# Kernel tuning notes

Hardware: AMD Instinct MI355X
Metric: run time of the kernel (lower is better)

The kernel has to match this reference:

```python
import jax, jax.numpy as jnp
import numpy as np

N = 4
SEGMENTS = 16
IN_F = 256
OUT_F = 256
BATCH = 512


def chebyshev_lobatto(n):
    # Chebyshev-Lobatto interpolation nodes on [-1, 1]
    k = jnp.arange(n, dtype=jnp.float32)
    return -jnp.cos(jnp.pi * k / (n - 1))


def lagrange_basis(x, nodes):
    # x: [B, In]; returns basis values [B, In, n]
    n = nodes.shape[0]
    cols = []
    for j in range(n):  # n is a small static constant (4)
        terms = [(x - nodes[m]) / (nodes[j] - nodes[m]) for m in range(n) if m != j]
        cols.append(jnp.prod(jnp.stack(terms, axis=0), axis=0))
    return jnp.stack(cols, axis=-1)


def setup_inputs() -> dict:
    key = jax.random.key(0)
    k1, k2 = jax.random.split(key)
    x = jax.random.uniform(k1, (BATCH, IN_F), dtype=jnp.float32, minval=-1.0, maxval=1.0)
    w = jax.random.uniform(
        k2, (OUT_F, IN_F, (N - 1) * SEGMENTS + 1), dtype=jnp.float32, minval=-1.0, maxval=1.0
    )
    return {"x": x, "w": w, "n": N, "segments": SEGMENTS}


def reference(x, w, n, segments):
    nodes = chebyshev_lobatto(n)
    # segment id per element, clamped to [0, segments-1]
    id_min = jnp.clip(((x + 1.0) / 2.0 * segments).astype(jnp.int32), 0, segments - 1)
    id_max = id_min + 1
    wid_min = id_min * (n - 1)  # start of weight slice; slice length == n
    # segment boundaries in x-space: eta(i) = i/segments * 2 - 1
    x_min = id_min.astype(x.dtype) / segments * 2.0 - 1.0
    x_max = id_max.astype(x.dtype) / segments * 2.0 - 1.0
    # rescale x into [-1, 1] within its segment
    x_in = 2.0 * (x - x_min) / (x_max - x_min) - 1.0
    basis = lagrange_basis(x_in, nodes)  # [B, In, n]
    # gather per-element weight slice: w_g[b,i,j,o] = w[o, i, wid_min[b,i]+j]
    idx = wid_min[..., None] + jnp.arange(n)  # [B, In, n]
    w_t = jnp.transpose(w, (1, 2, 0))  # [In, K, Out]
    in_f = w.shape[1]
    w_g = w_t[jnp.arange(in_f)[None, :, None], idx]  # [B, In, n, Out]
    # interpolate and sum over in_features (matches einsum 'ijk,jkli->jl')
    return jnp.einsum("bin,bino->bo", basis, w_g)
```

## Files before the change

kernel.cpp:

```cpp
#include <hip/hip_runtime.h>


typedef _Float16 h2 __attribute__((ext_vector_type(2)));

#define INF     256
#define OUTF    256
#define WSTRIDE 49
#define OSTRIDE (INF * WSTRIDE)
#define NSPLIT  32
#define IPB     8
#define WE_UINTS (256 * 256 * 32)

#define GLOAD16(gptr, lptr)                                                         \
  __builtin_amdgcn_global_load_lds(                                                 \
      (const __attribute__((address_space(1))) unsigned int*)(gptr),                \
      (__attribute__((address_space(3))) unsigned int*)(lptr), 16, 0, 0)

__global__ __launch_bounds__(256)
void pp_expand(const float* __restrict__ w, unsigned int* __restrict__ we) {
    const int i = blockIdx.x;
    const int o = threadIdx.x;
    const float* src = w + (size_t)o * OSTRIDE + i * WSTRIDE;
    float t[49];
    #pragma unroll
    for (int k = 0; k < 49; ++k) t[k] = src[k];
    unsigned int pk[32];
    #pragma unroll
    for (int s = 0; s < 16; ++s) {
        auto p0 = __builtin_amdgcn_cvt_pkrtz(t[3*s],   t[3*s+1]);
        auto p1 = __builtin_amdgcn_cvt_pkrtz(t[3*s+2], t[3*s+3]);
        pk[2*s]   = __builtin_bit_cast(unsigned int, p0);
        pk[2*s+1] = __builtin_bit_cast(unsigned int, p1);
    }
    uint4* dst = (uint4*)(we + ((size_t)i * 256 + o) * 32);
    #pragma unroll
    for (int k = 0; k < 8; ++k)
        dst[k] = make_uint4(pk[4*k], pk[4*k+1], pk[4*k+2], pk[4*k+3]);
}

#define STAGE(ci)                                                                   \
do {                                                                                \
    unsigned int* lds_ = &smem[((ci) & 1) * 4096];                                  \
    _Pragma("unroll")                                                               \
    for (int it = 0; it < 4; ++it) {                                                \
        int f_ = it * 256 + tid;                            \
        int iloc_ = f_ >> 9;                                                        \
        int rem_  = f_ & 511;                                                       \
        const unsigned int* gp_ = we + ((size_t)(i_base + (ci)*2 + iloc_) * 256     \
                                        + o_base) * 32 + rem_ * 4;                  \
        GLOAD16(gp_, lds_ + f_ * 4);                                                \
    }                                                                               \
} while (0)

#define COMPUTE(ci)                                                                 \
do {                                                                                \
    _Pragma("unroll")                                                               \
    for (int il = 0; il < 2; ++il) {                                                \
        const int ig_ = (ci) * 2 + il;                                              \
        const unsigned int* p_ = &smem[((ci) & 1) * 4096                            \
                                       + (il * 64 + o_off) * 32 + sseg[ig_] * 2];   \
        const h2 cA_ = ch01[ig_], cB_ = ch23[ig_];                                  \
        _Pragma("unroll")                                                           \
        for (int oo = 0; oo < 16; ++oo) {                                           \
            uint2 v_ = *(const uint2*)(p_ + oo * 32);                               \
            acc[oo] = __builtin_amdgcn_fdot2(__builtin_bit_cast(h2, v_.x), cA_,     \
                                             acc[oo], false);                       \
            acc[oo] = __builtin_amdgcn_fdot2(__builtin_bit_cast(h2, v_.y), cB_,     \
                                             acc[oo], false);                       \
        }                                                                           \
    }                                                                               \
} while (0)

__global__ __launch_bounds__(256, 4)
void pp_partial(const float* __restrict__ x, const unsigned int* __restrict__ we,
                float* __restrict__ part) {
    __shared__ unsigned int smem[8192];

    const int tid  = threadIdx.x;
    const int wave = tid >> 6, lane = tid & 63;
    const int isplit = blockIdx.x;
    const int i_base = isplit * IPB;
    const int o_base = blockIdx.y * 64;
    const int b_base = blockIdx.z * 64;
    const int b = b_base + lane;
    const int o_off = wave * 16;

    int sseg[IPB];
    h2  ch01[IPB], ch23[IPB];
    {
        const float4* xp = (const float4*)(x + (size_t)b * INF + i_base);
        float4 x0 = xp[0], x1 = xp[1];
        float xs[8] = {x0.x, x0.y, x0.z, x0.w, x1.x, x1.y, x1.z, x1.w};
        #pragma unroll
        for (int i = 0; i < IPB; ++i) {
            float xx = xs[i];
            int id = (int)((xx + 1.0f) * 8.0f);
            id = id < 0 ? 0 : (id > 15 ? 15 : id);
            float u = (xx - ((float)id * 0.125f - 1.0f)) * 16.0f - 1.0f;
            float a = u + 1.0f, b2 = u + 0.5f, cc = u - 0.5f, d = u - 1.0f;
            float c0 = b2 * cc * d  * (-2.0f / 3.0f);
            float c1 = a  * cc * d  * ( 4.0f / 3.0f);
            float c2 = a  * b2 * d  * (-4.0f / 3.0f);
            float c3 = a  * b2 * cc * ( 2.0f / 3.0f);
            h2 pA; pA[0] = (_Float16)c0; pA[1] = (_Float16)c1;
            h2 pB; pB[0] = (_Float16)c2; pB[1] = (_Float16)c3;
            ch01[i] = pA; ch23[i] = pB;
            sseg[i] = id;
        }
    }

    float acc[16];
    #pragma unroll
    for (int q = 0; q < 16; ++q) acc[q] = 0.0f;

    STAGE(0);
    __syncthreads();
    STAGE(1); COMPUTE(0); __syncthreads();
    STAGE(2); COMPUTE(1); __syncthreads();
    STAGE(3); COMPUTE(2); __syncthreads();
    COMPUTE(3);

    float4* wp = (float4*)(part + (size_t)isplit * (512 * 256)
                                + (size_t)b * 256 + o_base + o_off);
    #pragma unroll
    for (int q = 0; q < 4; ++q)
        wp[q] = make_float4(acc[4*q], acc[4*q+1], acc[4*q+2], acc[4*q+3]);
}

__global__ __launch_bounds__(256)
void pp_reduce(const float* __restrict__ part, float* __restrict__ out) {
    const size_t off = (size_t)blockIdx.x * 256 + threadIdx.x;
    float s = 0.0f;
    #pragma unroll
    for (int k = 0; k < NSPLIT; ++k)
        s += part[(size_t)k * (512 * 256) + off];
    out[off] = s;
}

extern "C" void kernel_launch(void* const* d_in, const int* in_sizes, int n_in,
                              void* d_out, int out_size, void* d_ws, size_t ws_size,
                              hipStream_t stream) {
    const float* x = (const float*)d_in[0];
    const float* w = (const float*)d_in[1];
    float* out = (float*)d_out;
    unsigned int* we = (unsigned int*)d_ws;
    float* part = (float*)((char*)d_ws + (size_t)WE_UINTS * 4);
    (void)ws_size; (void)n_in; (void)in_sizes; (void)out_size;

    pp_expand<<<dim3(256), 256, 0, stream>>>(w, we);
    pp_partial<<<dim3(NSPLIT, 4, 8), 256, 0, stream>>>(x, we, part);
    pp_reduce<<<dim3(512), 256, 0, stream>>>(part, out);
}
```

Before: 91.75 us.

## Interleave output pairs in fp16 weight layout and load whole tile once

The expand kernel now stores weights with two adjacent outputs interleaved per segment, so each compute lane reads one 16-byte LDS vector that serves two outputs. The partial kernel drops the double-buffered staging pipeline and loads all 8 inputs' weights for 32 outputs at once. It then transposes the accumulators through LDS so the partial-sum stores are coalesced. The grid doubles in the output dimension, and the reduce kernel is vectorised to float4. The change trades the load/compute overlap for fewer LDS instructions and better store coalescing.

```diff
diff --git a/kernel.cpp b/kernel.cpp
--- a/kernel.cpp
+++ b/kernel.cpp
@@ -9,7 +9,7 @@
 #define OSTRIDE (INF * WSTRIDE)
 #define NSPLIT  32
 #define IPB     8
-#define WE_UINTS (256 * 256 * 32)
+#define WE_UINTS (256 * 128 * 64)
 
 #define GLOAD16(gptr, lptr)                                                         \
   __builtin_amdgcn_global_load_lds(                                                 \
@@ -24,52 +24,18 @@
     float t[49];
     #pragma unroll
     for (int k = 0; k < 49; ++k) t[k] = src[k];
-    unsigned int pk[32];
+    const int op = o >> 1, e = o & 1;
+    unsigned int* dst = we + ((size_t)i * 128 + op) * 64 + e * 2;
     #pragma unroll
     for (int s = 0; s < 16; ++s) {
         auto p0 = __builtin_amdgcn_cvt_pkrtz(t[3*s],   t[3*s+1]);
         auto p1 = __builtin_amdgcn_cvt_pkrtz(t[3*s+2], t[3*s+3]);
-        pk[2*s]   = __builtin_bit_cast(unsigned int, p0);
-        pk[2*s+1] = __builtin_bit_cast(unsigned int, p1);
+        uint2 v;
+        v.x = __builtin_bit_cast(unsigned int, p0);
+        v.y = __builtin_bit_cast(unsigned int, p1);
+        *(uint2*)(dst + s * 4) = v;
     }
-    uint4* dst = (uint4*)(we + ((size_t)i * 256 + o) * 32);
-    #pragma unroll
-    for (int k = 0; k < 8; ++k)
-        dst[k] = make_uint4(pk[4*k], pk[4*k+1], pk[4*k+2], pk[4*k+3]);
 }
-
-#define STAGE(ci)                                                                   \
-do {                                                                                \
-    unsigned int* lds_ = &smem[((ci) & 1) * 4096];                                  \
-    _Pragma("unroll")                                                               \
-    for (int it = 0; it < 4; ++it) {                                                \
-        int f_ = it * 256 + tid;                            \
-        int iloc_ = f_ >> 9;                                                        \
-        int rem_  = f_ & 511;                                                       \
-        const unsigned int* gp_ = we + ((size_t)(i_base + (ci)*2 + iloc_) * 256     \
-                                        + o_base) * 32 + rem_ * 4;                  \
-        GLOAD16(gp_, lds_ + f_ * 4);                                                \
-    }                                                                               \
-} while (0)
-
-#define COMPUTE(ci)                                                                 \
-do {                                                                                \
-    _Pragma("unroll")                                                               \
-    for (int il = 0; il < 2; ++il) {                                                \
-        const int ig_ = (ci) * 2 + il;                                              \
-        const unsigned int* p_ = &smem[((ci) & 1) * 4096                            \
-                                       + (il * 64 + o_off) * 32 + sseg[ig_] * 2];   \
-        const h2 cA_ = ch01[ig_], cB_ = ch23[ig_];                                  \
-        _Pragma("unroll")                                                           \
-        for (int oo = 0; oo < 16; ++oo) {                                           \
-            uint2 v_ = *(const uint2*)(p_ + oo * 32);                               \
-            acc[oo] = __builtin_amdgcn_fdot2(__builtin_bit_cast(h2, v_.x), cA_,     \
-                                             acc[oo], false);                       \
-            acc[oo] = __builtin_amdgcn_fdot2(__builtin_bit_cast(h2, v_.y), cB_,     \
-                                             acc[oo], false);                       \
-        }                                                                           \
-    }                                                                               \
-} while (0)
 
 __global__ __launch_bounds__(256, 4)
 void pp_partial(const float* __restrict__ x, const unsigned int* __restrict__ we,
@@ -78,15 +44,23 @@
 
     const int tid  = threadIdx.x;
     const int wave = tid >> 6, lane = tid & 63;
-    const int isplit = blockIdx.x;
-    const int i_base = isplit * IPB;
-    const int o_base = blockIdx.y * 64;
-    const int b_base = blockIdx.z * 64;
+    const int isplit  = blockIdx.x;
+    const int i_base  = isplit * IPB;
+    const int op_base = blockIdx.y * 16;
+    const int o_base  = blockIdx.y * 32;
+    const int b_base  = blockIdx.z * 64;
     const int b = b_base + lane;
-    const int o_off = wave * 16;
 
-    int sseg[IPB];
-    h2  ch01[IPB], ch23[IPB];
+    #pragma unroll
+    for (int it = 0; it < 8; ++it) {
+        int u = it * 256 + tid;
+        int iloc = u >> 8, opl = (u >> 4) & 15, s = u & 15;
+        const unsigned int* gp =
+            we + (((size_t)(i_base + iloc) * 128 + op_base + opl) * 16 + s) * 4;
+        GLOAD16(gp, &smem[u * 4]);
+    }
+
+    int sseg[IPB]; h2 cA[IPB], cB[IPB];
     {
         const float4* xp = (const float4*)(x + (size_t)b * INF + i_base);
         float4 x0 = xp[0], x1 = xp[1];
@@ -104,37 +78,66 @@
             float c3 = a  * b2 * cc * ( 2.0f / 3.0f);
             h2 pA; pA[0] = (_Float16)c0; pA[1] = (_Float16)c1;
             h2 pB; pB[0] = (_Float16)c2; pB[1] = (_Float16)c3;
-            ch01[i] = pA; ch23[i] = pB;
-            sseg[i] = id;
+            cA[i] = pA; cB[i] = pB; sseg[i] = id;
         }
     }
 
-    float acc[16];
+    __syncthreads();
+
+    float acc[8];
     #pragma unroll
-    for (int q = 0; q < 16; ++q) acc[q] = 0.0f;
+    for (int q = 0; q < 8; ++q) acc[q] = 0.0f;
 
-    STAGE(0);
+    #pragma unroll
+    for (int i = 0; i < IPB; ++i) {
+        const unsigned int* p = &smem[(i * 16 + wave * 4) * 64 + sseg[i] * 4];
+        #pragma unroll
+        for (int pq = 0; pq < 4; ++pq) {
+            uint4 v = *(const uint4*)(p + pq * 64);
+            acc[2*pq]   = __builtin_amdgcn_fdot2(__builtin_bit_cast(h2, v.x), cA[i],
+                                                 acc[2*pq],   false);
+            acc[2*pq]   = __builtin_amdgcn_fdot2(__builtin_bit_cast(h2, v.y), cB[i],
+                                                 acc[2*pq],   false);
+            acc[2*pq+1] = __builtin_amdgcn_fdot2(__builtin_bit_cast(h2, v.z), cA[i],
+                                                 acc[2*pq+1], false);
+            acc[2*pq+1] = __builtin_amdgcn_fdot2(__builtin_bit_cast(h2, v.w), cB[i],
+                                                 acc[2*pq+1], false);
+        }
+    }
+
     __syncthreads();
-    STAGE(1); COMPUTE(0); __syncthreads();
-    STAGE(2); COMPUTE(1); __syncthreads();
-    STAGE(3); COMPUTE(2); __syncthreads();
-    COMPUTE(3);
+    float* smf = (float*)smem;
+    #pragma unroll
+    for (int q = 0; q < 8; ++q)
+        smf[lane * 33 + wave * 8 + q] = acc[q];
+    __syncthreads();
 
-    float4* wp = (float4*)(part + (size_t)isplit * (512 * 256)
-                                + (size_t)b * 256 + o_base + o_off);
+    const int qo = tid & 7;
+    const int g  = tid >> 3;
     #pragma unroll
-    for (int q = 0; q < 4; ++q)
-        wp[q] = make_float4(acc[4*q], acc[4*q+1], acc[4*q+2], acc[4*q+3]);
+    for (int r = 0; r < 2; ++r) {
+        int b_l = g + 32 * r;
+        float4 v;
+        v.x = smf[b_l * 33 + qo * 4 + 0];
+        v.y = smf[b_l * 33 + qo * 4 + 1];
+        v.z = smf[b_l * 33 + qo * 4 + 2];
+        v.w = smf[b_l * 33 + qo * 4 + 3];
+        *(float4*)(part + (size_t)isplit * (512 * 256)
+                        + (size_t)(b_base + b_l) * 256 + o_base + qo * 4) = v;
+    }
 }
 
 __global__ __launch_bounds__(256)
 void pp_reduce(const float* __restrict__ part, float* __restrict__ out) {
-    const size_t off = (size_t)blockIdx.x * 256 + threadIdx.x;
-    float s = 0.0f;
+    const size_t off4 = (size_t)blockIdx.x * 256 + threadIdx.x;
+    const float4* p4 = (const float4*)part;
+    float4 s = make_float4(0.f, 0.f, 0.f, 0.f);
     #pragma unroll
-    for (int k = 0; k < NSPLIT; ++k)
-        s += part[(size_t)k * (512 * 256) + off];
-    out[off] = s;
+    for (int k = 0; k < NSPLIT; ++k) {
+        float4 v = p4[(size_t)k * (512 * 64) + off4];
+        s.x += v.x; s.y += v.y; s.z += v.z; s.w += v.w;
+    }
+    ((float4*)out)[off4] = s;
 }
 
 extern "C" void kernel_launch(void* const* d_in, const int* in_sizes, int n_in,
@@ -148,6 +151,6 @@
     (void)ws_size; (void)n_in; (void)in_sizes; (void)out_size;
 
     pp_expand<<<dim3(256), 256, 0, stream>>>(w, we);
-    pp_partial<<<dim3(NSPLIT, 4, 8), 256, 0, stream>>>(x, we, part);
-    pp_reduce<<<dim3(512), 256, 0, stream>>>(part, out);
+    pp_partial<<<dim3(NSPLIT, 8, 8), 256, 0, stream>>>(x, we, part);
+    pp_reduce<<<dim3(128), 256, 0, stream>>>(part, out);
 }
```

Measured after the change: 85.19 us. 1.08x faster.
